# Performance work log

Hardware: AMD Instinct MI355X
Metric: run time of the kernel (lower is better)

Reference implementation:

```python
import jax, jax.numpy as jnp
import numpy as np

B, N1, N2, C, P, H, MLP = 8, 4096, 4096, 512, 256, 8, 2048
HD = C // H  # head dim = 64
EPS = 1e-12


def _l2norm(x):
    # torch F.normalize(dim=-1): x / max(||x||_2, eps)
    n = jnp.sqrt(jnp.sum(x * x, axis=-1, keepdims=True))
    return x / jnp.maximum(n, EPS)


def setup_inputs() -> dict:
    key = jax.random.key(0)
    ks = jax.random.split(key, 8)
    w = lambda i, shape: jax.random.normal(ks[i], shape, jnp.float32) * 0.02
    return {
        "x1": jax.random.normal(ks[0], (B, N1, C), jnp.float32),
        "x2": jax.random.normal(ks[1], (B, N2, C), jnp.float32),
        "Wq": w(2, (C, C)), "bq": jnp.zeros((C,), jnp.float32),
        "Wkv": w(3, (C, 2 * C)), "bkv": jnp.zeros((2 * C,), jnp.float32),
        # proj_k and proj_v share ONE Linear(N_2, proj_size) in the source
        "Wp": w(4, (N2, P)), "bp": jnp.zeros((P,), jnp.float32),
        "pos_q": jnp.zeros((1, N1, C), jnp.float32),
        "pos_k": jnp.zeros((1, N2, C), jnp.float32),
        "temperature": jnp.ones((H, 1, 1), jnp.float32),
        "W1": w(5, (C, MLP)), "b1": jnp.zeros((MLP,), jnp.float32),
        "W2": w(6, (MLP, C)), "b2": jnp.zeros((C,), jnp.float32),
    }


def reference(x1, x2, Wq, bq, Wkv, bkv, Wp, bp, pos_q, pos_k, temperature,
              W1, b1, W2, b2):
    # q += pos_embed_q is in-place in torch, so q_skip includes pos embedding
    q = x1 @ Wq + bq + pos_q                      # [B,N1,C]
    q_skip = q
    kv = x2 @ Wkv + bkv                           # [B,N2,2C]
    k = kv[..., :C] + pos_k                       # [B,N2,C]
    v = kv[..., C:]                               # [B,N2,C]

    qh = q.reshape(B, N1, H, HD).transpose(0, 2, 1, 3)   # [B,H,N1,hd]
    kh = k.reshape(B, N2, H, HD).transpose(0, 2, 1, 3)   # [B,H,N2,hd]
    vh = v.reshape(B, N2, H, HD).transpose(0, 2, 1, 3)   # [B,H,N2,hd]

    # project K^T and V^T along the sequence axis (shared weights)
    kp = jnp.einsum('bhnd,np->bhdp', kh, Wp) + bp        # [B,H,hd,P]
    vp_t = jnp.einsum('bhnd,np->bhdp', vh, Wp) + bp      # [B,H,hd,P]

    attn = jnp.einsum('bhqd,bhdp->bhqp', qh, kp) * temperature  # [B,H,N1,P]
    attn = jax.nn.softmax(attn, axis=-1)                 # dropout: eval mode

    x = jnp.einsum('bhqp,bhdp->bhqd', attn, vp_t)        # [B,H,N1,hd]
    # source does permute(0,3,1,2).reshape(B,N1,C) -- replicate exactly
    x = x.transpose(0, 3, 1, 2).reshape(B, N1, C)

    x = _l2norm(x + q_skip)                              # Add & L2-Norm
    h = jax.nn.gelu(x @ W1 + b1, approximate=False)      # nn.GELU (exact)
    out = _l2norm(h @ W2 + b2 + x)                       # FFN -> Add & L2-Norm
    return out
```

## Files before the change

kernel.cpp:

```cpp
#include <hip/hip_runtime.h>
#include <hip/hip_bf16.h>
#include <math.h>

#define B_    8
#define N1_   4096
#define N2_   4096
#define C_    512
#define P_    256
#define H_    8
#define MLP_  2048
#define HD_   64

typedef __hip_bfloat16 bf16;
typedef __attribute__((ext_vector_type(8))) short short8;
typedef __attribute__((ext_vector_type(4))) float f32x4;

__device__ __forceinline__ float bf2f(bf16 v) { return __bfloat162float(v); }
__device__ __forceinline__ bf16  f2bf(float v) { return __float2bfloat16(v); }
__device__ __forceinline__ float ubf2f(unsigned short u) {
  union { float f; unsigned int i; } cv; cv.i = ((unsigned int)u) << 16; return cv.f;
}
__device__ __forceinline__ unsigned short f2bfu(float v) {
  union { bf16 b; unsigned short u; } cv; cv.b = __float2bfloat16(v); return cv.u;
}
__device__ __forceinline__ float gelu_exact(float x) {
  return 0.5f * x * (1.0f + erff(x * 0.70710678118654752f));
}

__device__ __forceinline__ void gload16(const void* g, void* l) {
  __builtin_amdgcn_global_load_lds(
      (const __attribute__((address_space(1))) void*)g,
      (__attribute__((address_space(3))) void*)l, 16, 0, 0);
}

__global__ __launch_bounds__(256) void f2b_kernel(
    const float* __restrict__ in, bf16* __restrict__ out, int n4)
{
  int i = blockIdx.x * 256 + threadIdx.x;
  const int stride = gridDim.x * 256;
  for (; i < n4; i += stride) {
    const float4 v = ((const float4*)in)[i];
    ushort4 o;
    o.x = f2bfu(v.x); o.y = f2bfu(v.y); o.z = f2bfu(v.z); o.w = f2bfu(v.w);
    ((ushort4*)out)[i] = o;
  }
}

__global__ __launch_bounds__(256) void transpose_f2b_kernel(
    const float* __restrict__ in, bf16* __restrict__ out, int K, int N, int ldin)
{
  __shared__ float tile[32][33];
  const int kb = blockIdx.y * 32, nb = blockIdx.x * 32;
  const int tx = threadIdx.x & 31, ty = threadIdx.x >> 5;
  #pragma unroll
  for (int i = 0; i < 4; ++i)
    tile[ty + 8 * i][tx] = in[(size_t)(kb + ty + 8 * i) * ldin + nb + tx];
  __syncthreads();
  #pragma unroll
  for (int i = 0; i < 4; ++i)
    out[(size_t)(nb + ty + 8 * i) * K + kb + tx] = f2bf(tile[tx][ty + 8 * i]);
}

__global__ __launch_bounds__(256) void transpose_bf16_kernel(
    const bf16* __restrict__ in, bf16* __restrict__ out, int R, int Cc)
{
  __shared__ unsigned short tile[64][80];
  const size_t ib = (size_t)blockIdx.z * R * Cc;
  const int rb = blockIdx.y * 64, cb = blockIdx.x * 64;
  const int tr = threadIdx.x >> 3, ch = threadIdx.x & 7;
  #pragma unroll
  for (int p = 0; p < 2; ++p) {
    const int r = tr + 32 * p;
    const short8 v = *(const short8*)(in + ib + (size_t)(rb + r) * Cc + cb + ch * 8);
    *(short8*)&tile[r][ch * 8] = v;
  }
  __syncthreads();
  #pragma unroll
  for (int p = 0; p < 2; ++p) {
    const int c = tr + 32 * p;
    short8 v;
    #pragma unroll
    for (int e = 0; e < 8; ++e) v[e] = (short)tile[ch * 8 + e][c];
    *(short8*)(out + ib + (size_t)(cb + c) * R + rb + ch * 8) = v;
  }
}

template<int BN, int OUTF32, int ACT, int POS>
__global__ __launch_bounds__(256) void mfma_gemm_kernel(
    const bf16* __restrict__ A, const bf16* __restrict__ Bt,
    const float* __restrict__ bias, const float* __restrict__ pos, int posmask,
    void* __restrict__ Cv, int M, int N, int K)
{
  constexpr int WGN = BN / 64;
  constexpr int WGR = 4 / WGN;
  constexpr int FM  = 128 / (16 * WGR);
  __shared__ bf16 As[128 * 32];
  __shared__ bf16 Bs[BN * 32];
  const int t  = threadIdx.x;
  const int l  = t & 63;
  const int w  = t >> 6;
  const int wr = w / WGN, wc = w % WGN;
  const int lr = l & 15, kg = l >> 4;

  const int gx  = gridDim.x;
  const int nwg = gx * gridDim.y;
  const int h   = blockIdx.y * gx + blockIdx.x;
  int bx = blockIdx.x, by = blockIdx.y;
  if ((nwg & 7) == 0) {
    const int tid = (h & 7) * (nwg >> 3) + (h >> 3);
    bx = tid % gx; by = tid / gx;
  }
  const int m0 = by * 128, n0 = bx * BN;

  const bf16* ga = A  + (size_t)(m0 + (t >> 2)) * K + (t & 3) * 8;
  const bf16* gb = Bt + (size_t)(n0 + (t >> 2)) * K + (t & 3) * 8;
  char* asl = (char*)As + t * 16;
  char* bsl = (char*)Bs + t * 16;

  f32x4 acc[FM][4] = {};

  for (int k0 = 0; k0 < K; k0 += 32) {
    gload16(ga, asl);
    gload16(ga + (size_t)64 * K, asl + 4096);
    gload16(gb, bsl);
    if (BN == 128) gload16(gb + (size_t)64 * K, bsl + 4096);
    ga += 32; gb += 32;
    __syncthreads();
    short8 af[FM], bfv[4];
    #pragma unroll
    for (int i = 0; i < FM; ++i)
      af[i] = *(const short8*)&As[(wr * (FM * 16) + i * 16 + lr) * 32 + kg * 8];
    #pragma unroll
    for (int j = 0; j < 4; ++j)
      bfv[j] = *(const short8*)&Bs[(wc * 64 + j * 16 + lr) * 32 + kg * 8];
    #pragma unroll
    for (int i = 0; i < FM; ++i)
      #pragma unroll
      for (int j = 0; j < 4; ++j)
        acc[i][j] = __builtin_amdgcn_mfma_f32_16x16x32_bf16(
            af[i], bfv[j], acc[i][j], 0, 0, 0);
    __syncthreads();
  }

  #pragma unroll
  for (int i = 0; i < FM; ++i) {
    #pragma unroll
    for (int j = 0; j < 4; ++j) {
      const int n = n0 + wc * 64 + j * 16 + lr;
      const float bv = bias[n];
      #pragma unroll
      for (int r = 0; r < 4; ++r) {
        const int m = m0 + wr * (FM * 16) + i * 16 + kg * 4 + r;
        float v = acc[i][j][r] + bv;
        if (POS) v += pos[(size_t)(m & posmask) * N + n];
        if (ACT) v = gelu_exact(v);
        if (OUTF32) ((float*)Cv)[(size_t)m * N + n] = v;
        else        ((bf16*)Cv)[(size_t)m * N + n] = f2bf(v);
      }
    }
  }
}

template<int BIASM>
__global__ __launch_bounds__(256) void proj_kernel(
    const bf16* __restrict__ A, const bf16* __restrict__ Bt,
    const float* __restrict__ bias, bf16* __restrict__ Cb,
    int M, int N, int K, long aBatch, long bBatch, long cBatch)
{
  __shared__ bf16 As[64 * 32];
  __shared__ bf16 Bs[64 * 32];
  const int t = threadIdx.x, l = t & 63, w = t >> 6;
  const int wr = w >> 1, wc = w & 1;
  const int lr = l & 15, kg = l >> 4;
  const int z = blockIdx.z;
  const int m0 = blockIdx.y * 64, n0 = blockIdx.x * 64;
  const bf16* ga = A  + (size_t)z * aBatch + (size_t)(m0 + (t >> 2)) * K + (t & 3) * 8;
  const bf16* gb = Bt + (size_t)z * bBatch + (size_t)(n0 + (t >> 2)) * K + (t & 3) * 8;
  char* asl = (char*)As + t * 16;
  char* bsl = (char*)Bs + t * 16;
  f32x4 acc[2][2] = {};
  for (int k0 = 0; k0 < K; k0 += 32) {
    gload16(ga, asl);
    gload16(gb, bsl);
    ga += 32; gb += 32;
    __syncthreads();
    short8 af[2], bfr[2];
    #pragma unroll
    for (int i = 0; i < 2; ++i)
      af[i] = *(const short8*)&As[(wr * 32 + i * 16 + lr) * 32 + kg * 8];
    #pragma unroll
    for (int j = 0; j < 2; ++j)
      bfr[j] = *(const short8*)&Bs[(wc * 32 + j * 16 + lr) * 32 + kg * 8];
    #pragma unroll
    for (int i = 0; i < 2; ++i)
      #pragma unroll
      for (int j = 0; j < 2; ++j)
        acc[i][j] = __builtin_amdgcn_mfma_f32_16x16x32_bf16(
            af[i], bfr[j], acc[i][j], 0, 0, 0);
    __syncthreads();
  }
  #pragma unroll
  for (int i = 0; i < 2; ++i)
    #pragma unroll
    for (int j = 0; j < 2; ++j) {
      const int n = n0 + wc * 32 + j * 16 + lr;
      #pragma unroll
      for (int r = 0; r < 4; ++r) {
        const int m = m0 + wr * 32 + i * 16 + kg * 4 + r;
        const float v = acc[i][j][r] + (BIASM ? bias[m] : bias[n]);
        Cb[(size_t)z * cBatch + (size_t)m * N + n] = f2bf(v);
      }
    }
}

__global__ __launch_bounds__(256) void attn_mfma_kernel(
    const bf16* __restrict__ qb, const bf16* __restrict__ kpT,
    const bf16* __restrict__ vp, const float* __restrict__ temp,
    bf16* __restrict__ xatT)
{
  __shared__ bf16 qs[64 * 64];
  __shared__ bf16 us[256 * 64];
  __shared__ bf16 vs[64 * 256];
  const int t = threadIdx.x, w = t >> 6, l = t & 63;
  const int lr = l & 15, kg = l >> 4;
  const int b = blockIdx.z, h = blockIdx.y;
  const int q0 = blockIdx.x * 64;
  const int bh = b * H_ + h;
  const float tv = temp[h];

  {
    const int rowb = t >> 3, ch = t & 7;
    #pragma unroll
    for (int p = 0; p < 2; ++p) {
      const int r = rowb + 32 * p;
      const short8 v = *(const short8*)(qb + ((size_t)(b * N1_ + q0 + r)) * C_ + h * HD_ + ch * 8);
      *(short8*)((char*)qs + ((r * 128 + ch * 16) ^ ((r & 7) << 4))) = v;
    }
    const bf16* kpb = kpT + (size_t)bh * (P_ * HD_);
    #pragma unroll
    for (int p = 0; p < 8; ++p) {
      const int r = rowb + 32 * p;
      const short8 v = *(const short8*)(kpb + r * HD_ + ch * 8);
      *(short8*)((char*)us + ((r * 128 + ch * 16) ^ ((r & 7) << 4))) = v;
    }
    const bf16* vpb = vp + (size_t)bh * (HD_ * P_);
    const int rowv = t >> 5, chv = t & 31;
    #pragma unroll
    for (int p = 0; p < 8; ++p) {
      const int r = rowv + 8 * p;
      const short8 v = *(const short8*)(vpb + r * P_ + chv * 8);
      *(short8*)((char*)vs + ((r * 512 + chv * 16) ^ ((r & 7) << 4))) = v;
    }
  }
  __syncthreads();

  short8 aq[2];
  {
    const int row = w * 16 + lr;
    const int sw = (row & 7) << 4;
    aq[0] = *(const short8*)((const char*)qs + ((row * 128 +  0 + kg * 16) ^ sw));
    aq[1] = *(const short8*)((const char*)qs + ((row * 128 + 64 + kg * 16) ^ sw));
  }
  f32x4 s[16] = {};
  #pragma unroll
  for (int j = 0; j < 16; ++j) {
    const int row = j * 16 + lr;
    const int sw = (row & 7) << 4;
    const short8 b0 = *(const short8*)((const char*)us + ((row * 128 +  0 + kg * 16) ^ sw));
    const short8 b1 = *(const short8*)((const char*)us + ((row * 128 + 64 + kg * 16) ^ sw));
    s[j] = __builtin_amdgcn_mfma_f32_16x16x32_bf16(aq[0], b0, s[j], 0, 0, 0);
    s[j] = __builtin_amdgcn_mfma_f32_16x16x32_bf16(aq[1], b1, s[j], 0, 0, 0);
  }

  float inv_[4];
  #pragma unroll
  for (int j = 0; j < 16; ++j)
    #pragma unroll
    for (int r = 0; r < 4; ++r) s[j][r] *= tv;
  #pragma unroll
  for (int r = 0; r < 4; ++r) {
    float m = s[0][r];
    #pragma unroll
    for (int j = 1; j < 16; ++j) m = fmaxf(m, s[j][r]);
    #pragma unroll
    for (int off = 1; off < 16; off <<= 1) m = fmaxf(m, __shfl_xor(m, off));
    float sum = 0.f;
    #pragma unroll
    for (int j = 0; j < 16; ++j) { s[j][r] = __expf(s[j][r] - m); sum += s[j][r]; }
    #pragma unroll
    for (int off = 1; off < 16; off <<= 1) sum += __shfl_xor(sum, off);
    inv_[r] = 1.0f / sum;
  }
  __syncthreads();

  #pragma unroll
  for (int r = 0; r < 4; ++r) {
    const int q = w * 16 + kg * 4 + r;
    const int sw = (q & 7) << 4;
    #pragma unroll
    for (int j = 0; j < 16; ++j) {
      const int p = j * 16 + lr;
      ((unsigned short*)us)[((q * 512 + p * 2) ^ sw) >> 1] = f2bfu(s[j][r] * inv_[r]);
    }
  }
  __syncthreads();

  f32x4 o[4] = {};
  #pragma unroll
  for (int kc = 0; kc < 8; ++kc) {
    const int qrow = w * 16 + lr;
    const short8 pb = *(const short8*)((const char*)us +
        ((qrow * 512 + kc * 64 + kg * 16) ^ ((qrow & 7) << 4)));
    #pragma unroll
    for (int i = 0; i < 4; ++i) {
      const int drow = i * 16 + lr;
      const short8 vb = *(const short8*)((const char*)vs +
          ((drow * 512 + kc * 64 + kg * 16) ^ ((drow & 7) << 4)));
      o[i] = __builtin_amdgcn_mfma_f32_16x16x32_bf16(vb, pb, o[i], 0, 0, 0);
    }
  }
  const int qq = q0 + w * 16 + lr;
  bf16* ob = xatT + (size_t)bh * (HD_ * (size_t)N1_) + qq;
  #pragma unroll
  for (int i = 0; i < 4; ++i)
    #pragma unroll
    for (int r = 0; r < 4; ++r) {
      const int d = i * 16 + kg * 4 + r;
      ob[(size_t)d * N1_] = f2bf(o[i][r]);
    }
}

__global__ __launch_bounds__(256) void norm1_kernel(
    const bf16* __restrict__ xatT, const bf16* __restrict__ qb,
    bf16* __restrict__ xb)
{
  const int row = blockIdx.x;
  const int b = row >> 12, np = row & 4095;
  const int d = np >> 6, h = (np >> 3) & 7, qhi = np & 7;
  const int c = threadIdx.x * 2;
  const size_t tbase = ((size_t)(b * H_ + h) * HD_ + d) * N1_ + qhi * 512 + c;
  const size_t qbase = (size_t)row * C_ + c;
  const ushort2 xa = *(const ushort2*)((const unsigned short*)xatT + tbase);
  const ushort2 qa = *(const ushort2*)((const unsigned short*)qb + qbase);
  float v0 = ubf2f(xa.x) + ubf2f(qa.x);
  float v1 = ubf2f(xa.y) + ubf2f(qa.y);
  float ss = v0 * v0 + v1 * v1;
  #pragma unroll
  for (int off = 32; off > 0; off >>= 1) ss += __shfl_xor(ss, off);
  __shared__ float sw[4];
  if ((threadIdx.x & 63) == 0) sw[threadIdx.x >> 6] = ss;
  __syncthreads();
  const float tot = sw[0] + sw[1] + sw[2] + sw[3];
  const float scale = 1.0f / fmaxf(sqrtf(tot), 1e-12f);
  ushort2 o;
  o.x = f2bfu(v0 * scale);
  o.y = f2bfu(v1 * scale);
  *(ushort2*)((unsigned short*)xb + qbase) = o;
}

__global__ __launch_bounds__(256) void norm2_kernel(
    const float* __restrict__ yb, const bf16* __restrict__ xb,
    float* __restrict__ outp)
{
  const int row = blockIdx.x;
  const int c0 = threadIdx.x, c1 = threadIdx.x + 256;
  float v0 = yb[(size_t)row * C_ + c0] + bf2f(xb[(size_t)row * C_ + c0]);
  float v1 = yb[(size_t)row * C_ + c1] + bf2f(xb[(size_t)row * C_ + c1]);
  float ss = v0 * v0 + v1 * v1;
  #pragma unroll
  for (int off = 32; off > 0; off >>= 1) ss += __shfl_xor(ss, off);
  __shared__ float sw[4];
  if ((threadIdx.x & 63) == 0) sw[threadIdx.x >> 6] = ss;
  __syncthreads();
  const float tot = sw[0] + sw[1] + sw[2] + sw[3];
  const float scale = 1.0f / fmaxf(sqrtf(tot), 1e-12f);
  outp[(size_t)row * C_ + c0] = v0 * scale;
  outp[(size_t)row * C_ + c1] = v1 * scale;
}

extern "C" void kernel_launch(void* const* d_in, const int* in_sizes, int n_in,
                              void* d_out, int out_size, void* d_ws, size_t ws_size,
                              hipStream_t stream)
{
  const float* x1   = (const float*)d_in[0];
  const float* x2   = (const float*)d_in[1];
  const float* Wq   = (const float*)d_in[2];
  const float* bq   = (const float*)d_in[3];
  const float* Wkv  = (const float*)d_in[4];
  const float* bkv  = (const float*)d_in[5];
  const float* Wp   = (const float*)d_in[6];
  const float* bp   = (const float*)d_in[7];
  const float* posq = (const float*)d_in[8];
  const float* posk = (const float*)d_in[9];
  const float* temp = (const float*)d_in[10];
  const float* W1   = (const float*)d_in[11];
  const float* b1   = (const float*)d_in[12];
  const float* W2   = (const float*)d_in[13];
  const float* b2   = (const float*)d_in[14];

  char* ws = (char*)d_ws;
  bf16*  Abuf = (bf16*)(ws);
  bf16*  Bbuf = (bf16*)(ws + 33554432);
  bf16*  Cbuf = (bf16*)(ws + 67108864);
  bf16*  kpT  = (bf16*)(ws + 100663296);
  bf16*  vpb  = (bf16*)(ws + 102760448);
  bf16*  WpT  = (bf16*)(ws + 104857600);
  bf16*  Wqt  = (bf16*)(ws + 106954752);
  bf16*  Wkt  = (bf16*)(ws + 107479040);
  bf16*  Wvt  = (bf16*)(ws + 108003328);
  float* outp = (float*)d_out;

  int CH;
  size_t w1t_off, w2t_off, yb_off;
  if (ws_size >= 239075328UL) {
    CH = 32768; w1t_off = 167772160UL; w2t_off = 169869312UL; yb_off = 171966464UL;
  } else if (ws_size >= 138412032UL) {
    CH = 16384; w1t_off = 100663296UL; w2t_off = 102760448UL; yb_off = 104857600UL;
  } else {
    CH = 8192;  w1t_off = 100663296UL; w2t_off = 102760448UL; yb_off = 106954752UL;
  }
  bf16*  W1t = (bf16*)(ws + w1t_off);
  bf16*  W2t = (bf16*)(ws + w2t_off);
  float* yb  = (float*)(ws + yb_off);

  const dim3 blk(256);
  const int Mrows = B_ * N1_;
  bf16* xatT = Bbuf;
  bf16* xb   = Abuf;
  bf16* hb   = Bbuf;
  bf16* qb   = Cbuf;

  f2b_kernel<<<dim3(2048), blk, 0, stream>>>(x2, Abuf, (B_ * N2_ * C_) / 4);
  transpose_f2b_kernel<<<dim3(16, 16), blk, 0, stream>>>(Wkv,      Wkt, C_, C_, 2 * C_);
  transpose_f2b_kernel<<<dim3(16, 16), blk, 0, stream>>>(Wkv + C_, Wvt, C_, C_, 2 * C_);
  transpose_f2b_kernel<<<dim3(16, 16), blk, 0, stream>>>(Wq,       Wqt, C_, C_, C_);
  transpose_f2b_kernel<<<dim3(8, 128), blk, 0, stream>>>(Wp,       WpT, N2_, P_, P_);

  mfma_gemm_kernel<128,0,0,1><<<dim3(C_/128, Mrows/128), blk, 0, stream>>>(
      Abuf, Wkt, bkv, posk, N2_ - 1, Bbuf, Mrows, C_, C_);
  transpose_bf16_kernel<<<dim3(C_/64, N2_/64, B_), blk, 0, stream>>>(
      Bbuf, Cbuf, N2_, C_);
  proj_kernel<1><<<dim3(1, 4, B_*H_), blk, 0, stream>>>(
      WpT, Cbuf, bp, kpT, P_, HD_, N2_, 0L, (long)HD_*N2_, (long)P_*HD_);
  mfma_gemm_kernel<128,0,0,0><<<dim3(C_/128, Mrows/128), blk, 0, stream>>>(
      Abuf, Wvt, bkv + C_, nullptr, 0, Bbuf, Mrows, C_, C_);
  transpose_bf16_kernel<<<dim3(C_/64, N2_/64, B_), blk, 0, stream>>>(
      Bbuf, Cbuf, N2_, C_);
  proj_kernel<0><<<dim3(4, 1, B_*H_), blk, 0, stream>>>(
      Cbuf, WpT, bp, vpb, HD_, P_, N2_, (long)HD_*N2_, 0L, (long)HD_*P_);
  f2b_kernel<<<dim3(2048), blk, 0, stream>>>(x1, Abuf, (B_ * N1_ * C_) / 4);
  mfma_gemm_kernel<128,0,0,1><<<dim3(C_/128, Mrows/128), blk, 0, stream>>>(
      Abuf, Wqt, bq, posq, N1_ - 1, qb, Mrows, C_, C_);
  attn_mfma_kernel<<<dim3(N1_/64, H_, B_), blk, 0, stream>>>(
      qb, kpT, vpb, temp, xatT);
  transpose_f2b_kernel<<<dim3(64, 16), blk, 0, stream>>>(W1, W1t, C_,   MLP_, MLP_);
  transpose_f2b_kernel<<<dim3(16, 64), blk, 0, stream>>>(W2, W2t, MLP_, C_,   C_);
  norm1_kernel<<<dim3(Mrows), blk, 0, stream>>>(xatT, qb, xb);
  for (int c = 0; c < Mrows / CH; ++c) {
    const bf16* xc = xb + (size_t)c * CH * C_;
    mfma_gemm_kernel<128,0,1,0><<<dim3(MLP_/128, CH/128), blk, 0, stream>>>(
        xc, W1t, b1, nullptr, 0, hb, CH, MLP_, C_);
    mfma_gemm_kernel<64,1,0,0><<<dim3(C_/64, CH/128), blk, 0, stream>>>(
        hb, W2t, b2, nullptr, 0, yb, CH, C_, MLP_);
    norm2_kernel<<<dim3(CH), blk, 0, stream>>>(
        yb, xc, outp + (size_t)c * CH * C_);
  }
}
```

Measured before the change: 783.9 us.

## Fuse K/V transposes into GEMM epilogue, fast GELU, wider W2 tile

The K and V projection GEMMs now write their output directly in transposed [B,C,N2] layout from the epilogue, which removes the two separate transpose_bf16 kernels and their round trip through global memory. Exact erf-based GELU is replaced with the Abramowitz-Stegun polynomial approximation using a hardware reciprocal and fast exp. The second FFN GEMM switches from a 64-wide to a 128-wide N tile. The transposed stores are 8-byte column-strided writes, which may coalesce poorly, and the GELU approximation adds a small numerical error.

Result: no change. 773.4 us (-1.3%).

```diff
diff --git a/kernel.cpp b/kernel.cpp
--- a/kernel.cpp
+++ b/kernel.cpp
@@ -23,8 +23,18 @@
 __device__ __forceinline__ unsigned short f2bfu(float v) {
   union { bf16 b; unsigned short u; } cv; cv.b = __float2bfloat16(v); return cv.u;
 }
-__device__ __forceinline__ float gelu_exact(float x) {
-  return 0.5f * x * (1.0f + erff(x * 0.70710678118654752f));
+__device__ __forceinline__ float gelu_fast(float x) {
+  const float u = fabsf(x) * 0.70710678118654752f;
+  const float t = __builtin_amdgcn_rcpf(__builtin_fmaf(0.3275911f, u, 1.0f));
+  float p = __builtin_fmaf(1.061405429f, t, -1.453152027f);
+  p = __builtin_fmaf(p, t, 1.421413741f);
+  p = __builtin_fmaf(p, t, -0.284496736f);
+  p = __builtin_fmaf(p, t, 0.254829592f);
+  p *= t;
+  const float e = __expf(-u * u);
+  float erfv = __builtin_fmaf(-p, e, 1.0f);
+  erfv = (x < 0.0f) ? -erfv : erfv;
+  return 0.5f * x * (1.0f + erfv);
 }
 
 __device__ __forceinline__ void gload16(const void* g, void* l) {
@@ -61,31 +71,7 @@
     out[(size_t)(nb + ty + 8 * i) * K + kb + tx] = f2bf(tile[tx][ty + 8 * i]);
 }
 
-__global__ __launch_bounds__(256) void transpose_bf16_kernel(
-    const bf16* __restrict__ in, bf16* __restrict__ out, int R, int Cc)
-{
-  __shared__ unsigned short tile[64][80];
-  const size_t ib = (size_t)blockIdx.z * R * Cc;
-  const int rb = blockIdx.y * 64, cb = blockIdx.x * 64;
-  const int tr = threadIdx.x >> 3, ch = threadIdx.x & 7;
-  #pragma unroll
-  for (int p = 0; p < 2; ++p) {
-    const int r = tr + 32 * p;
-    const short8 v = *(const short8*)(in + ib + (size_t)(rb + r) * Cc + cb + ch * 8);
-    *(short8*)&tile[r][ch * 8] = v;
-  }
-  __syncthreads();
-  #pragma unroll
-  for (int p = 0; p < 2; ++p) {
-    const int c = tr + 32 * p;
-    short8 v;
-    #pragma unroll
-    for (int e = 0; e < 8; ++e) v[e] = (short)tile[ch * 8 + e][c];
-    *(short8*)(out + ib + (size_t)(cb + c) * R + rb + ch * 8) = v;
-  }
-}
-
-template<int BN, int OUTF32, int ACT, int POS>
+template<int BN, int OUTF32, int ACT, int POS, int TRANSC>
 __global__ __launch_bounds__(256) void mfma_gemm_kernel(
     const bf16* __restrict__ A, const bf16* __restrict__ Bt,
     const float* __restrict__ bias, const float* __restrict__ pos, int posmask,
@@ -148,14 +134,27 @@
     for (int j = 0; j < 4; ++j) {
       const int n = n0 + wc * 64 + j * 16 + lr;
       const float bv = bias[n];
-      #pragma unroll
-      for (int r = 0; r < 4; ++r) {
-        const int m = m0 + wr * (FM * 16) + i * 16 + kg * 4 + r;
-        float v = acc[i][j][r] + bv;
-        if (POS) v += pos[(size_t)(m & posmask) * N + n];
-        if (ACT) v = gelu_exact(v);
-        if (OUTF32) ((float*)Cv)[(size_t)m * N + n] = v;
-        else        ((bf16*)Cv)[(size_t)m * N + n] = f2bf(v);
+      if (TRANSC) {
+        const int mb = m0 + wr * (FM * 16) + i * 16 + kg * 4;
+        ushort4 pk;
+        #pragma unroll
+        for (int r = 0; r < 4; ++r) {
+          const int m = mb + r;
+          float v = acc[i][j][r] + bv;
+          if (POS) v += pos[(size_t)(m & posmask) * N + n];
+          ((unsigned short*)&pk)[r] = f2bfu(v);
+        }
+        *(ushort4*)&((bf16*)Cv)[((size_t)(mb >> 12) * N + n) * (size_t)N1_ + (mb & 4095)] = pk;
+      } else {
+        #pragma unroll
+        for (int r = 0; r < 4; ++r) {
+          const int m = m0 + wr * (FM * 16) + i * 16 + kg * 4 + r;
+          float v = acc[i][j][r] + bv;
+          if (POS) v += pos[(size_t)(m & posmask) * N + n];
+          if (ACT) v = gelu_fast(v);
+          if (OUTF32) ((float*)Cv)[(size_t)m * N + n] = v;
+          else        ((bf16*)Cv)[(size_t)m * N + n] = f2bf(v);
+        }
       }
     }
   }
@@ -436,20 +435,16 @@
   transpose_f2b_kernel<<<dim3(16, 16), blk, 0, stream>>>(Wq,       Wqt, C_, C_, C_);
   transpose_f2b_kernel<<<dim3(8, 128), blk, 0, stream>>>(Wp,       WpT, N2_, P_, P_);
 
-  mfma_gemm_kernel<128,0,0,1><<<dim3(C_/128, Mrows/128), blk, 0, stream>>>(
-      Abuf, Wkt, bkv, posk, N2_ - 1, Bbuf, Mrows, C_, C_);
-  transpose_bf16_kernel<<<dim3(C_/64, N2_/64, B_), blk, 0, stream>>>(
-      Bbuf, Cbuf, N2_, C_);
+  mfma_gemm_kernel<128,0,0,1,1><<<dim3(C_/128, Mrows/128), blk, 0, stream>>>(
+      Abuf, Wkt, bkv, posk, N2_ - 1, Cbuf, Mrows, C_, C_);
   proj_kernel<1><<<dim3(1, 4, B_*H_), blk, 0, stream>>>(
       WpT, Cbuf, bp, kpT, P_, HD_, N2_, 0L, (long)HD_*N2_, (long)P_*HD_);
-  mfma_gemm_kernel<128,0,0,0><<<dim3(C_/128, Mrows/128), blk, 0, stream>>>(
-      Abuf, Wvt, bkv + C_, nullptr, 0, Bbuf, Mrows, C_, C_);
-  transpose_bf16_kernel<<<dim3(C_/64, N2_/64, B_), blk, 0, stream>>>(
-      Bbuf, Cbuf, N2_, C_);
+  mfma_gemm_kernel<128,0,0,0,1><<<dim3(C_/128, Mrows/128), blk, 0, stream>>>(
+      Abuf, Wvt, bkv + C_, nullptr, 0, Cbuf, Mrows, C_, C_);
   proj_kernel<0><<<dim3(4, 1, B_*H_), blk, 0, stream>>>(
       Cbuf, WpT, bp, vpb, HD_, P_, N2_, (long)HD_*N2_, 0L, (long)HD_*P_);
   f2b_kernel<<<dim3(2048), blk, 0, stream>>>(x1, Abuf, (B_ * N1_ * C_) / 4);
-  mfma_gemm_kernel<128,0,0,1><<<dim3(C_/128, Mrows/128), blk, 0, stream>>>(
+  mfma_gemm_kernel<128,0,0,1,0><<<dim3(C_/128, Mrows/128), blk, 0, stream>>>(
       Abuf, Wqt, bq, posq, N1_ - 1, qb, Mrows, C_, C_);
   attn_mfma_kernel<<<dim3(N1_/64, H_, B_), blk, 0, stream>>>(
       qb, kpT, vpb, temp, xatT);
@@ -458,9 +453,9 @@
   norm1_kernel<<<dim3(Mrows), blk, 0, stream>>>(xatT, qb, xb);
   for (int c = 0; c < Mrows / CH; ++c) {
     const bf16* xc = xb + (size_t)c * CH * C_;
-    mfma_gemm_kernel<128,0,1,0><<<dim3(MLP_/128, CH/128), blk, 0, stream>>>(
+    mfma_gemm_kernel<128,0,1,0,0><<<dim3(MLP_/128, CH/128), blk, 0, stream>>>(
         xc, W1t, b1, nullptr, 0, hb, CH, MLP_, C_);
-    mfma_gemm_kernel<64,1,0,0><<<dim3(C_/64, CH/128), blk, 0, stream>>>(
+    mfma_gemm_kernel<128,1,0,0,0><<<dim3(C_/128, CH/128), blk, 0, stream>>>(
         hb, W2t, b2, nullptr, 0, yb, CH, C_, MLP_);
     norm2_kernel<<<dim3(CH), blk, 0, stream>>>(
         yb, xc, outp + (size_t)c * CH * C_);
```
